# Optimization experiments

Measured on AMD Instinct MI355X. Metric: run time of the kernel, lower is better.

Reference implementation:

```python
import jax, jax.numpy as jnp
import numpy as np

N = 50000
E = 800000
IN_DIM = 128
HID = 32
HEADS = 4
OUT_DIM = 32
NEG_SLOPE = 0.2


def setup_inputs() -> dict:
    key = jax.random.key(0)
    ks = jax.random.split(key, 10)
    x = jax.random.normal(ks[0], (N, IN_DIM), dtype=jnp.float32)
    edge_index = jax.random.randint(ks[1], (2, E), 0, N, dtype=jnp.int64)
    # layer 1: in 128 -> 4 heads x 32, concat
    W1 = jax.random.normal(ks[2], (IN_DIM, HEADS * HID), dtype=jnp.float32) * (1.0 / np.sqrt(IN_DIM))
    a_src1 = jax.random.normal(ks[3], (HEADS, HID), dtype=jnp.float32) * 0.1
    a_dst1 = jax.random.normal(ks[4], (HEADS, HID), dtype=jnp.float32) * 0.1
    b1 = jnp.zeros((HEADS * HID,), dtype=jnp.float32)
    # layer 2: in 128 -> 1 head x 32, mean
    W2 = jax.random.normal(ks[5], (HEADS * HID, OUT_DIM), dtype=jnp.float32) * (1.0 / np.sqrt(HEADS * HID))
    a_src2 = jax.random.normal(ks[6], (1, OUT_DIM), dtype=jnp.float32) * 0.1
    a_dst2 = jax.random.normal(ks[7], (1, OUT_DIM), dtype=jnp.float32) * 0.1
    b2 = jnp.zeros((OUT_DIM,), dtype=jnp.float32)
    return {"x": x, "edge_index": edge_index, "W1": W1, "a_src1": a_src1,
            "a_dst1": a_dst1, "b1": b1, "W2": W2, "a_src2": a_src2,
            "a_dst2": a_dst2, "b2": b2}


def gat_layer(x, src, dst, W, a_src, a_dst, b, heads, concat, num_nodes):
    # linear transform -> [N, H, C]
    h = (x @ W).reshape(num_nodes, heads, -1)
    # per-node attention halves, gathered per edge -> [E, H]
    alpha = jax.nn.leaky_relu((h * a_src).sum(-1)[src] + (h * a_dst).sum(-1)[dst],
                              negative_slope=NEG_SLOPE)
    # segment softmax over edges grouped by destination node
    seg_max = jax.ops.segment_max(alpha, dst, num_segments=num_nodes)
    e = jnp.exp(alpha - seg_max[dst])
    denom = jax.ops.segment_sum(e, dst, num_segments=num_nodes)[dst]
    w = e / jnp.maximum(denom, 1e-16)
    # weighted message scatter-sum -> [N, H, C]
    out = jax.ops.segment_sum(h[src] * w[..., None], dst, num_segments=num_nodes)
    out = out.reshape(num_nodes, -1) if concat else out.mean(axis=1)
    return out + b


def reference(x, edge_index, W1, a_src1, a_dst1, b1, W2, a_src2, a_dst2, b2):
    num_nodes = x.shape[0]
    loops = jnp.arange(num_nodes, dtype=edge_index.dtype)
    src = jnp.concatenate([edge_index[0], loops])  # add self-loops (PyG default)
    dst = jnp.concatenate([edge_index[1], loops])
    h = jax.nn.relu(gat_layer(x, src, dst, W1, a_src1, a_dst1, b1, HEADS, True, num_nodes))
    out = gat_layer(h, src, dst, W2, a_src2, a_dst2, b2, 1, False, num_nodes)
    return jax.nn.sigmoid(out)
```

## Files before the change

kernel.cpp:

```cpp
#include <hip/hip_runtime.h>
#include <math.h>

#define NN 50000
#define NE 800000
#define NT (NN + NE)
#define SCAN_BLOCKS 196

__device__ __forceinline__ float lrelu(float a) { return a > 0.f ? a : 0.2f * a; }

__device__ __forceinline__ float sel4(float4 v, int h) {
  float r = v.x;
  r = (h == 1) ? v.y : r;
  r = (h == 2) ? v.z : r;
  r = (h == 3) ? v.w : r;
  return r;
}

__device__ __forceinline__ unsigned int f2bf(float f) {
  unsigned int u = __float_as_uint(f);
  return (u + 0x7FFFu + ((u >> 16) & 1u)) >> 16;
}
__device__ __forceinline__ unsigned int packbf(float lo, float hi) {
  return f2bf(lo) | (f2bf(hi) << 16);
}
__device__ __forceinline__ float bflo(unsigned int v) { return __uint_as_float(v << 16); }
__device__ __forceinline__ float bfhi(unsigned int v) { return __uint_as_float(v & 0xFFFF0000u); }

__global__ void k_detect(const unsigned int* __restrict__ eb, int* __restrict__ flag) {
  __shared__ int nz;
  if (threadIdx.x == 0) nz = 0;
  __syncthreads();
  int local = 0;
  for (int i = threadIdx.x; i < 2048; i += 256) local |= (eb[2 * i + 1] != 0u);
  if (local) nz = 1;
  __syncthreads();
  if (threadIdx.x == 0) *flag = (nz == 0) ? 1 : 0;
}

__global__ __launch_bounds__(256) void k_pass1(const void* __restrict__ eb,
                                               const int* __restrict__ flag,
                                               int* __restrict__ cnt,
                                               unsigned int* __restrict__ pw) {
  int e0 = (blockIdx.x * 256 + threadIdx.x) * 4;
  if (e0 >= NT) return;
  int is64 = *flag;
  int d0, d1, d2, d3;
  if (e0 < NE) {
    if (is64) {
      const uint4* p = (const uint4*)((const unsigned int*)eb + 2 * ((size_t)NE + e0));
      uint4 a = p[0], b = p[1];
      d0 = (int)a.x; d1 = (int)a.z; d2 = (int)b.x; d3 = (int)b.z;
    } else {
      int4 v = *(const int4*)((const int*)eb + (size_t)NE + e0);
      d0 = v.x; d1 = v.y; d2 = v.z; d3 = v.w;
    }
  } else {
    d0 = e0 - NE; d1 = d0 + 1; d2 = d0 + 2; d3 = d0 + 3;
  }
  unsigned int p0 = (unsigned int)atomicAdd(&cnt[d0], 1);
  unsigned int p1 = (unsigned int)atomicAdd(&cnt[d1], 1);
  unsigned int p2 = (unsigned int)atomicAdd(&cnt[d2], 1);
  unsigned int p3 = (unsigned int)atomicAdd(&cnt[d3], 1);
  *(uint4*)&pw[e0] = make_uint4(p0, p1, p2, p3);
}

__global__ __launch_bounds__(256) void k_bsum(const int* __restrict__ cnt,
                                              int* __restrict__ bsum) {
  int i = blockIdx.x * 256 + threadIdx.x;
  int v = (i < NN) ? cnt[i] : 0;
#pragma unroll
  for (int off = 1; off < 64; off <<= 1) v += __shfl_xor(v, off, 64);
  __shared__ int ws[4];
  int lane = threadIdx.x & 63, wid = threadIdx.x >> 6;
  if (lane == 0) ws[wid] = v;
  __syncthreads();
  if (threadIdx.x == 0) bsum[blockIdx.x] = ws[0] + ws[1] + ws[2] + ws[3];
}

__global__ __launch_bounds__(256) void k_bscan(const int* __restrict__ bsum,
                                               int* __restrict__ boff,
                                               int* __restrict__ rowp) {
  int t = threadIdx.x;
  int lane = t & 63, wid = t >> 6;
  int v = (t < SCAN_BLOCKS) ? bsum[t] : 0;
  int incl = v;
#pragma unroll
  for (int off = 1; off < 64; off <<= 1) {
    int u = __shfl_up(incl, off, 64);
    if (lane >= off) incl += u;
  }
  __shared__ int wsum[4], woff[4];
  if (lane == 63) wsum[wid] = incl;
  __syncthreads();
  if (t == 0) {
    woff[0] = 0;
    woff[1] = wsum[0];
    woff[2] = wsum[0] + wsum[1];
    woff[3] = wsum[0] + wsum[1] + wsum[2];
  }
  __syncthreads();
  if (t < SCAN_BLOCKS) boff[t] = woff[wid] + incl - v;
  if (t == 0) rowp[NN] = NT;
}

__global__ __launch_bounds__(256) void k_rowp(const int* __restrict__ cnt,
                                              const int* __restrict__ boff,
                                              int* __restrict__ rowp) {
  int i = blockIdx.x * 256 + threadIdx.x;
  int t = threadIdx.x;
  int lane = t & 63, wid = t >> 6;
  int v = (i < NN) ? cnt[i] : 0;
  int incl = v;
#pragma unroll
  for (int off = 1; off < 64; off <<= 1) {
    int u = __shfl_up(incl, off, 64);
    if (lane >= off) incl += u;
  }
  __shared__ int wsum[4], woff[4];
  if (lane == 63) wsum[wid] = incl;
  __syncthreads();
  if (t == 0) {
    woff[0] = 0;
    woff[1] = wsum[0];
    woff[2] = wsum[0] + wsum[1];
    woff[3] = wsum[0] + wsum[1] + wsum[2];
  }
  __syncthreads();
  if (i < NN) rowp[i] = boff[blockIdx.x] + woff[wid] + incl - v;
}

__global__ __launch_bounds__(256) void k_pass2(const void* __restrict__ eb,
                                               const int* __restrict__ flag,
                                               const int* __restrict__ rowp,
                                               const unsigned int* __restrict__ pw,
                                               int* __restrict__ csr) {
  int e0 = (blockIdx.x * 256 + threadIdx.x) * 4;
  if (e0 >= NT) return;
  int is64 = *flag;
  int s0, s1, s2, s3, d0, d1, d2, d3;
  if (e0 < NE) {
    if (is64) {
      const uint4* ps = (const uint4*)((const unsigned int*)eb + 2 * (size_t)e0);
      uint4 a = ps[0], b = ps[1];
      s0 = (int)a.x; s1 = (int)a.z; s2 = (int)b.x; s3 = (int)b.z;
      const uint4* pd = (const uint4*)((const unsigned int*)eb + 2 * ((size_t)NE + e0));
      uint4 c = pd[0], d = pd[1];
      d0 = (int)c.x; d1 = (int)c.z; d2 = (int)d.x; d3 = (int)d.z;
    } else {
      int4 vs = *(const int4*)((const int*)eb + (size_t)e0);
      s0 = vs.x; s1 = vs.y; s2 = vs.z; s3 = vs.w;
      int4 vd = *(const int4*)((const int*)eb + (size_t)NE + e0);
      d0 = vd.x; d1 = vd.y; d2 = vd.z; d3 = vd.w;
    }
  } else {
    s0 = d0 = e0 - NE;
    s1 = d1 = d0 + 1;
    s2 = d2 = d0 + 2;
    s3 = d3 = d0 + 3;
  }
  uint4 pv = *(const uint4*)&pw[e0];
  csr[rowp[d0] + (int)pv.x] = s0;
  csr[rowp[d1] + (int)pv.y] = s1;
  csr[rowp[d2] + (int)pv.z] = s2;
  csr[rowp[d3] + (int)pv.w] = s3;
}

__global__ __launch_bounds__(256) void k_gemm1(const float* __restrict__ X,
                                               const float* __restrict__ W,
                                               const float* __restrict__ a_src,
                                               const float* __restrict__ a_dst,
                                               unsigned int* __restrict__ Hb,
                                               float* __restrict__ AS,
                                               float* __restrict__ AD) {
  __shared__ float xt[32 * 36];
  __shared__ float wt[32 * 132];
  int tid = threadIdx.x;
  int tr = tid >> 6, tc = tid & 63;
  int r0 = blockIdx.x * 32;
  float acc[8][2];
#pragma unroll
  for (int i = 0; i < 8; ++i) {
    acc[i][0] = 0.f;
    acc[i][1] = 0.f;
  }

  for (int kb = 0; kb < 4; ++kb) {
    __syncthreads();
    {
      int row = tid >> 3, k4 = tid & 7;
      int gr = r0 + row;
      float4 v = make_float4(0.f, 0.f, 0.f, 0.f);
      if (gr < NN) v = ((const float4*)X)[(size_t)gr * 32 + kb * 8 + k4];
      xt[(k4 * 4 + 0) * 36 + row] = v.x;
      xt[(k4 * 4 + 1) * 36 + row] = v.y;
      xt[(k4 * 4 + 2) * 36 + row] = v.z;
      xt[(k4 * 4 + 3) * 36 + row] = v.w;
    }
#pragma unroll
    for (int i = tid; i < 1024; i += 256) {
      int kr = i >> 5, c4 = i & 31;
      *(float4*)&wt[kr * 132 + c4 * 4] = ((const float4*)W)[(size_t)(kb * 32 + kr) * 32 + c4];
    }
    __syncthreads();
#pragma unroll 4
    for (int k = 0; k < 32; ++k) {
      float4 xa = *(const float4*)&xt[k * 36 + tr * 8];
      float4 xb = *(const float4*)&xt[k * 36 + tr * 8 + 4];
      float2 wv = *(const float2*)&wt[k * 132 + tc * 2];
      float xr[8] = {xa.x, xa.y, xa.z, xa.w, xb.x, xb.y, xb.z, xb.w};
#pragma unroll
      for (int i = 0; i < 8; ++i) {
        acc[i][0] += xr[i] * wv.x;
        acc[i][1] += xr[i] * wv.y;
      }
    }
  }
  int head = tc >> 4;
  float2 sv = *(const float2*)&a_src[tc * 2];
  float2 dv = *(const float2*)&a_dst[tc * 2];
#pragma unroll
  for (int i = 0; i < 8; ++i) {
    int gr = r0 + tr * 8 + i;
    float ps = acc[i][0] * sv.x + acc[i][1] * sv.y;
    float pd = acc[i][0] * dv.x + acc[i][1] * dv.y;
#pragma unroll
    for (int off = 1; off < 16; off <<= 1) {
      ps += __shfl_xor(ps, off, 64);
      pd += __shfl_xor(pd, off, 64);
    }
    if (gr < NN) {
      Hb[(size_t)gr * 64 + tc] = packbf(acc[i][0], acc[i][1]);
      if ((tc & 15) == 0) {
        AS[gr * 4 + head] = ps;
        AD[gr * 4 + head] = pd;
      }
    }
  }
}

__global__ __launch_bounds__(256) void k_l1node(const int* __restrict__ rowp,
                                                const int* __restrict__ csr,
                                                const uint4* __restrict__ Hb,
                                                const float* __restrict__ AS,
                                                const float* __restrict__ AD,
                                                const float* __restrict__ b1,
                                                uint4* __restrict__ HMb) {
  int lane = threadIdx.x & 63, wid = threadIdx.x >> 6;
  int n = blockIdx.x * 4 + wid;
  if (n >= NN) return;
  int beg = rowp[n], end = rowp[n + 1];
  float4 ad4 = *(const float4*)&AD[n * 4];

  int sl = lane & 15;
  int g = lane >> 4;
  int hd = sl >> 2;
  float adh = sel4(ad4, hd);

  float a0 = 0.f, a1 = 0.f, a2 = 0.f, a3 = 0.f, a4 = 0.f, a5 = 0.f, a6 = 0.f, a7 = 0.f;
  float esum = 0.f;
  int i = beg + g;
  for (; i + 4 < end; i += 8) {
    int sA = csr[i];
    int sB = csr[i + 4];
    float lA = AS[sA * 4 + hd];
    float lB = AS[sB * 4 + hd];
    uint4 hA = Hb[(size_t)sA * 16 + sl];
    uint4 hB = Hb[(size_t)sB * 16 + sl];
    float wA = __expf(lrelu(lA + adh));
    float wB = __expf(lrelu(lB + adh));
    esum += wA + wB;
    a0 += wA * bflo(hA.x) + wB * bflo(hB.x);
    a1 += wA * bfhi(hA.x) + wB * bfhi(hB.x);
    a2 += wA * bflo(hA.y) + wB * bflo(hB.y);
    a3 += wA * bfhi(hA.y) + wB * bfhi(hB.y);
    a4 += wA * bflo(hA.z) + wB * bflo(hB.z);
    a5 += wA * bfhi(hA.z) + wB * bfhi(hB.z);
    a6 += wA * bflo(hA.w) + wB * bflo(hB.w);
    a7 += wA * bfhi(hA.w) + wB * bfhi(hB.w);
  }
  if (i < end) {
    int s = csr[i];
    float l = AS[s * 4 + hd];
    uint4 hv = Hb[(size_t)s * 16 + sl];
    float w0 = __expf(lrelu(l + adh));
    esum += w0;
    a0 += w0 * bflo(hv.x);
    a1 += w0 * bfhi(hv.x);
    a2 += w0 * bflo(hv.y);
    a3 += w0 * bfhi(hv.y);
    a4 += w0 * bflo(hv.z);
    a5 += w0 * bfhi(hv.z);
    a6 += w0 * bflo(hv.w);
    a7 += w0 * bfhi(hv.w);
  }
#pragma unroll
  for (int off = 16; off < 64; off <<= 1) {
    esum += __shfl_xor(esum, off, 64);
    a0 += __shfl_xor(a0, off, 64);
    a1 += __shfl_xor(a1, off, 64);
    a2 += __shfl_xor(a2, off, 64);
    a3 += __shfl_xor(a3, off, 64);
    a4 += __shfl_xor(a4, off, 64);
    a5 += __shfl_xor(a5, off, 64);
    a6 += __shfl_xor(a6, off, 64);
    a7 += __shfl_xor(a7, off, 64);
  }
  if (lane < 16) {
    float r = 1.f / esum;
    int c = sl * 8;
    float4 bva = *(const float4*)&b1[c];
    float4 bvb = *(const float4*)&b1[c + 4];
    float v0 = fmaxf(a0 * r + bva.x, 0.f);
    float v1 = fmaxf(a1 * r + bva.y, 0.f);
    float v2 = fmaxf(a2 * r + bva.z, 0.f);
    float v3 = fmaxf(a3 * r + bva.w, 0.f);
    float v4 = fmaxf(a4 * r + bvb.x, 0.f);
    float v5 = fmaxf(a5 * r + bvb.y, 0.f);
    float v6 = fmaxf(a6 * r + bvb.z, 0.f);
    float v7 = fmaxf(a7 * r + bvb.w, 0.f);
    HMb[(size_t)n * 16 + sl] =
        make_uint4(packbf(v0, v1), packbf(v2, v3), packbf(v4, v5), packbf(v6, v7));
  }
}

__global__ __launch_bounds__(256) void k_gemm2(const uint4* __restrict__ HMb,
                                               const float* __restrict__ W2,
                                               const float* __restrict__ a_src2,
                                               const float* __restrict__ a_dst2,
                                               uint4* __restrict__ Hb2,
                                               float* __restrict__ AS,
                                               float* __restrict__ AD) {
  __shared__ float wsm[128 * 32];
  int tid = threadIdx.x;
  for (int i = tid; i < 1024; i += 256) ((float4*)wsm)[i] = ((const float4*)W2)[i];
  __syncthreads();
  int rl = tid >> 2, sub = tid & 3;
  int r = blockIdx.x * 64 + rl;
  float acc[32];
#pragma unroll
  for (int j = 0; j < 32; ++j) acc[j] = 0.f;

  if (r < NN) {
    const uint4* xp = &HMb[(size_t)r * 16 + sub * 4];
    uint4 xq0 = xp[0], xq1 = xp[1], xq2 = xp[2], xq3 = xp[3];
    int kbase = sub * 32;
    unsigned int wds[16] = {xq0.x, xq0.y, xq0.z, xq0.w, xq1.x, xq1.y, xq1.z, xq1.w,
                            xq2.x, xq2.y, xq2.z, xq2.w, xq3.x, xq3.y, xq3.z, xq3.w};
#pragma unroll
    for (int t = 0; t < 16; ++t) {
      float xlo = bflo(wds[t]);
      float xhi = bfhi(wds[t]);
      const float4* wr0 = (const float4*)&wsm[(kbase + t * 2) * 32];
      const float4* wr1 = (const float4*)&wsm[(kbase + t * 2 + 1) * 32];
#pragma unroll
      for (int j4 = 0; j4 < 8; ++j4) {
        float4 w0 = wr0[j4];
        float4 w1 = wr1[j4];
        acc[j4 * 4 + 0] += xlo * w0.x + xhi * w1.x;
        acc[j4 * 4 + 1] += xlo * w0.y + xhi * w1.y;
        acc[j4 * 4 + 2] += xlo * w0.z + xhi * w1.z;
        acc[j4 * 4 + 3] += xlo * w0.w + xhi * w1.w;
      }
    }
  }
#pragma unroll
  for (int j = 0; j < 32; ++j) {
    acc[j] += __shfl_xor(acc[j], 1, 64);
    acc[j] += __shfl_xor(acc[j], 2, 64);
  }
  if (r < NN) {
    int c = sub * 8;
    float4 sv0 = ((const float4*)a_src2)[sub * 2];
    float4 sv1 = ((const float4*)a_src2)[sub * 2 + 1];
    float4 dv0 = ((const float4*)a_dst2)[sub * 2];
    float4 dv1 = ((const float4*)a_dst2)[sub * 2 + 1];
    float ps = acc[c + 0] * sv0.x + acc[c + 1] * sv0.y + acc[c + 2] * sv0.z +
               acc[c + 3] * sv0.w + acc[c + 4] * sv1.x + acc[c + 5] * sv1.y +
               acc[c + 6] * sv1.z + acc[c + 7] * sv1.w;
    float pd = acc[c + 0] * dv0.x + acc[c + 1] * dv0.y + acc[c + 2] * dv0.z +
               acc[c + 3] * dv0.w + acc[c + 4] * dv1.x + acc[c + 5] * dv1.y +
               acc[c + 6] * dv1.z + acc[c + 7] * dv1.w;
    ps += __shfl_xor(ps, 1, 64);
    ps += __shfl_xor(ps, 2, 64);
    pd += __shfl_xor(pd, 1, 64);
    pd += __shfl_xor(pd, 2, 64);
    Hb2[(size_t)r * 4 + sub] =
        make_uint4(packbf(acc[c + 0], acc[c + 1]), packbf(acc[c + 2], acc[c + 3]),
                   packbf(acc[c + 4], acc[c + 5]), packbf(acc[c + 6], acc[c + 7]));
    if (sub == 0) {
      AS[r] = ps;
      AD[r] = pd;
    }
  }
}

__global__ __launch_bounds__(256) void k_l2node(const int* __restrict__ rowp,
                                                const int* __restrict__ csr,
                                                const uint2* __restrict__ Hb2,
                                                const float* __restrict__ AS,
                                                const float* __restrict__ AD,
                                                const float* __restrict__ b2,
                                                float* __restrict__ out) {
  int lane = threadIdx.x & 63, wid = threadIdx.x >> 6;
  int n = blockIdx.x * 4 + wid;
  if (n >= NN) return;
  int beg = rowp[n], end = rowp[n + 1];
  float adn = AD[n];

  int sl = lane & 7;
  int g = lane >> 3;
  float a0 = 0.f, a1 = 0.f, a2 = 0.f, a3 = 0.f;
  float esum = 0.f;
  int i = beg + g;
  for (; i + 8 < end; i += 16) {
    int sA = csr[i];
    int sB = csr[i + 8];
    float lA = AS[sA];
    float lB = AS[sB];
    uint2 hA = Hb2[(size_t)sA * 8 + sl];
    uint2 hB = Hb2[(size_t)sB * 8 + sl];
    float wA = __expf(lrelu(lA + adn));
    float wB = __expf(lrelu(lB + adn));
    esum += wA + wB;
    a0 += wA * bflo(hA.x) + wB * bflo(hB.x);
    a1 += wA * bfhi(hA.x) + wB * bfhi(hB.x);
    a2 += wA * bflo(hA.y) + wB * bflo(hB.y);
    a3 += wA * bfhi(hA.y) + wB * bfhi(hB.y);
  }
  if (i < end) {
    int s = csr[i];
    float l = AS[s];
    uint2 hv = Hb2[(size_t)s * 8 + sl];
    float w0 = __expf(lrelu(l + adn));
    esum += w0;
    a0 += w0 * bflo(hv.x);
    a1 += w0 * bfhi(hv.x);
    a2 += w0 * bflo(hv.y);
    a3 += w0 * bfhi(hv.y);
  }
#pragma unroll
  for (int off = 8; off < 64; off <<= 1) {
    esum += __shfl_xor(esum, off, 64);
    a0 += __shfl_xor(a0, off, 64);
    a1 += __shfl_xor(a1, off, 64);
    a2 += __shfl_xor(a2, off, 64);
    a3 += __shfl_xor(a3, off, 64);
  }
  if (lane < 8) {
    float r = 1.f / esum;
    int c = sl * 4;
    float4 bv = *(const float4*)&b2[c];
    float vx = a0 * r + bv.x, vy = a1 * r + bv.y, vz = a2 * r + bv.z, vw = a3 * r + bv.w;
    *(float4*)&out[(size_t)n * 32 + c] =
        make_float4(1.f / (1.f + __expf(-vx)), 1.f / (1.f + __expf(-vy)),
                    1.f / (1.f + __expf(-vz)), 1.f / (1.f + __expf(-vw)));
  }
}

extern "C" void kernel_launch(void* const* d_in, const int* in_sizes, int n_in,
                              void* d_out, int out_size, void* d_ws, size_t ws_size,
                              hipStream_t stream) {
  (void)in_sizes; (void)n_in; (void)out_size; (void)ws_size;
  const float* x      = (const float*)d_in[0];
  const void*  eb     = d_in[1];
  const float* W1     = (const float*)d_in[2];
  const float* a_src1 = (const float*)d_in[3];
  const float* a_dst1 = (const float*)d_in[4];
  const float* b1     = (const float*)d_in[5];
  const float* W2     = (const float*)d_in[6];
  const float* a_src2 = (const float*)d_in[7];
  const float* a_dst2 = (const float*)d_in[8];
  const float* b2     = (const float*)d_in[9];
  float* out = (float*)d_out;

  char* w = (char*)d_ws;
  auto alloc = [&](size_t bytes) {
    char* p = w;
    w += (bytes + 255) & ~(size_t)255;
    return p;
  };
  int*          flag = (int*)alloc(4);
  int*          cnt  = (int*)alloc((size_t)NN * 4);
  int*          rowp = (int*)alloc((size_t)(NN + 1) * 4);
  unsigned int* pw   = (unsigned int*)alloc((size_t)NT * 4);
  int*          csr  = (int*)alloc((size_t)NT * 4);
  int*          bsum = (int*)alloc((size_t)SCAN_BLOCKS * 4);
  int*          boff = (int*)alloc((size_t)SCAN_BLOCKS * 4);
  uint4*        Hb1  = (uint4*)alloc((size_t)NN * 128 * 2);
  float*        AS1  = (float*)alloc((size_t)NN * 16);
  float*        AD1  = (float*)alloc((size_t)NN * 16);
  uint4*        HMb  = (uint4*)alloc((size_t)NN * 128 * 2);
  uint4* Hb2 = Hb1;
  float* AS2 = (float*)cnt;
  float* AD2 = (float*)pw;

  hipMemsetAsync(cnt, 0, (size_t)NN * 4, stream);
  k_detect<<<1, 256, 0, stream>>>((const unsigned int*)eb, flag);
  int egrid4 = (NT / 4 + 255) / 256;
  k_pass1<<<egrid4, 256, 0, stream>>>(eb, flag, cnt, pw);
  k_bsum<<<SCAN_BLOCKS, 256, 0, stream>>>(cnt, bsum);
  k_bscan<<<1, 256, 0, stream>>>(bsum, boff, rowp);
  k_rowp<<<SCAN_BLOCKS, 256, 0, stream>>>(cnt, boff, rowp);
  k_pass2<<<egrid4, 256, 0, stream>>>(eb, flag, rowp, pw, csr);

  k_gemm1<<<(NN + 31) / 32, 256, 0, stream>>>(x, W1, a_src1, a_dst1,
                                              (unsigned int*)Hb1, AS1, AD1);
  k_l1node<<<(NN + 3) / 4, 256, 0, stream>>>(rowp, csr, Hb1, AS1, AD1, b1, HMb);
  k_gemm2<<<(NN + 63) / 64, 256, 0, stream>>>(HMb, W2, a_src2, a_dst2, Hb2, AS2, AD2);
  k_l2node<<<(NN + 3) / 4, 256, 0, stream>>>(rowp, csr, (const uint2*)Hb2, AS2, AD2, b2, out);
}
```

Baseline: 275.1 us.

## Fuse layer-2 projection into layer-1 aggregation and drop detect/scan launches

The layer-1 neighbour aggregation kernel now also does the layer-2 linear transform and attention dot products in-wave, using W2 staged in shared memory. This removes the k_gemm2 launch and the full bf16 round-trip of the hidden activations through global memory. The separate edge-dtype detect kernel is replaced by a per-wave ballot probe inside the edge passes, and the single-block block-offset scan is folded into k_rowp, which cuts two more launches. In exchange, every 4-node block reloads the 16 KB W2 into LDS, which adds heavy redundant L2 traffic and LDS pressure and may limit occupancy.

```diff
diff --git a/kernel.cpp b/kernel.cpp
--- a/kernel.cpp
+++ b/kernel.cpp
@@ -26,26 +26,21 @@
 __device__ __forceinline__ float bflo(unsigned int v) { return __uint_as_float(v << 16); }
 __device__ __forceinline__ float bfhi(unsigned int v) { return __uint_as_float(v & 0xFFFF0000u); }
 
-__global__ void k_detect(const unsigned int* __restrict__ eb, int* __restrict__ flag) {
-  __shared__ int nz;
-  if (threadIdx.x == 0) nz = 0;
-  __syncthreads();
-  int local = 0;
-  for (int i = threadIdx.x; i < 2048; i += 256) local |= (eb[2 * i + 1] != 0u);
-  if (local) nz = 1;
-  __syncthreads();
-  if (threadIdx.x == 0) *flag = (nz == 0) ? 1 : 0;
+__device__ __forceinline__ int wave_is64(const void* eb, int wbase, int lane) {
+  unsigned int probe = ((const unsigned int*)eb)[2 * (size_t)(wbase + lane) + 1];
+  return (__ballot(probe != 0u) == 0ULL) ? 1 : 0;
 }
 
 __global__ __launch_bounds__(256) void k_pass1(const void* __restrict__ eb,
-                                               const int* __restrict__ flag,
                                                int* __restrict__ cnt,
                                                unsigned int* __restrict__ pw) {
   int e0 = (blockIdx.x * 256 + threadIdx.x) * 4;
   if (e0 >= NT) return;
-  int is64 = *flag;
+  int lane = threadIdx.x & 63;
   int d0, d1, d2, d3;
   if (e0 < NE) {
+    int wbase = (blockIdx.x * 256 + (threadIdx.x & ~63)) * 4;
+    int is64 = wave_is64(eb, wbase, lane);
     if (is64) {
       const uint4* p = (const uint4*)((const unsigned int*)eb + 2 * ((size_t)NE + e0));
       uint4 a = p[0], b = p[1];
@@ -77,68 +72,67 @@
   if (threadIdx.x == 0) bsum[blockIdx.x] = ws[0] + ws[1] + ws[2] + ws[3];
 }
 
-__global__ __launch_bounds__(256) void k_bscan(const int* __restrict__ bsum,
-                                               int* __restrict__ boff,
-                                               int* __restrict__ rowp) {
+__global__ __launch_bounds__(256) void k_rowp(const int* __restrict__ cnt,
+                                              const int* __restrict__ bsum,
+                                              int* __restrict__ rowp) {
+  __shared__ int pref[256];
+  __shared__ int wsum1[4], woff1[4];
   int t = threadIdx.x;
   int lane = t & 63, wid = t >> 6;
-  int v = (t < SCAN_BLOCKS) ? bsum[t] : 0;
+  {
+    int v = (t < SCAN_BLOCKS) ? bsum[t] : 0;
+    int incl = v;
+#pragma unroll
+    for (int off = 1; off < 64; off <<= 1) {
+      int u = __shfl_up(incl, off, 64);
+      if (lane >= off) incl += u;
+    }
+    if (lane == 63) wsum1[wid] = incl;
+    __syncthreads();
+    if (t == 0) {
+      woff1[0] = 0;
+      woff1[1] = wsum1[0];
+      woff1[2] = wsum1[0] + wsum1[1];
+      woff1[3] = wsum1[0] + wsum1[1] + wsum1[2];
+    }
+    __syncthreads();
+    pref[t] = woff1[wid] + incl - v;
+    __syncthreads();
+  }
+  int boffb = pref[blockIdx.x];
+  __shared__ int wsum2[4], woff2[4];
+  int i = blockIdx.x * 256 + t;
+  int v = (i < NN) ? cnt[i] : 0;
   int incl = v;
 #pragma unroll
   for (int off = 1; off < 64; off <<= 1) {
     int u = __shfl_up(incl, off, 64);
     if (lane >= off) incl += u;
   }
-  __shared__ int wsum[4], woff[4];
-  if (lane == 63) wsum[wid] = incl;
+  if (lane == 63) wsum2[wid] = incl;
   __syncthreads();
   if (t == 0) {
-    woff[0] = 0;
-    woff[1] = wsum[0];
-    woff[2] = wsum[0] + wsum[1];
-    woff[3] = wsum[0] + wsum[1] + wsum[2];
+    woff2[0] = 0;
+    woff2[1] = wsum2[0];
+    woff2[2] = wsum2[0] + wsum2[1];
+    woff2[3] = wsum2[0] + wsum2[1] + wsum2[2];
   }
   __syncthreads();
-  if (t < SCAN_BLOCKS) boff[t] = woff[wid] + incl - v;
-  if (t == 0) rowp[NN] = NT;
-}
-
-__global__ __launch_bounds__(256) void k_rowp(const int* __restrict__ cnt,
-                                              const int* __restrict__ boff,
-                                              int* __restrict__ rowp) {
-  int i = blockIdx.x * 256 + threadIdx.x;
-  int t = threadIdx.x;
-  int lane = t & 63, wid = t >> 6;
-  int v = (i < NN) ? cnt[i] : 0;
-  int incl = v;
-#pragma unroll
-  for (int off = 1; off < 64; off <<= 1) {
-    int u = __shfl_up(incl, off, 64);
-    if (lane >= off) incl += u;
-  }
-  __shared__ int wsum[4], woff[4];
-  if (lane == 63) wsum[wid] = incl;
-  __syncthreads();
-  if (t == 0) {
-    woff[0] = 0;
-    woff[1] = wsum[0];
-    woff[2] = wsum[0] + wsum[1];
-    woff[3] = wsum[0] + wsum[1] + wsum[2];
-  }
-  __syncthreads();
-  if (i < NN) rowp[i] = boff[blockIdx.x] + woff[wid] + incl - v;
+  if (i < NN) rowp[i] = boffb + woff2[wid] + incl - v;
+  if (blockIdx.x == 0 && t == 0) rowp[NN] = NT;
 }
 
 __global__ __launch_bounds__(256) void k_pass2(const void* __restrict__ eb,
-                                               const int* __restrict__ flag,
                                                const int* __restrict__ rowp,
                                                const unsigned int* __restrict__ pw,
                                                int* __restrict__ csr) {
   int e0 = (blockIdx.x * 256 + threadIdx.x) * 4;
   if (e0 >= NT) return;
-  int is64 = *flag;
+  int lane = threadIdx.x & 63;
   int s0, s1, s2, s3, d0, d1, d2, d3;
   if (e0 < NE) {
+    int wbase = (blockIdx.x * 256 + (threadIdx.x & ~63)) * 4;
+    int is64 = wave_is64(eb, wbase, lane);
     if (is64) {
       const uint4* ps = (const uint4*)((const unsigned int*)eb + 2 * (size_t)e0);
       uint4 a = ps[0], b = ps[1];
@@ -238,14 +232,24 @@
   }
 }
 
-__global__ __launch_bounds__(256) void k_l1node(const int* __restrict__ rowp,
-                                                const int* __restrict__ csr,
-                                                const uint4* __restrict__ Hb,
-                                                const float* __restrict__ AS,
-                                                const float* __restrict__ AD,
-                                                const float* __restrict__ b1,
-                                                uint4* __restrict__ HMb) {
-  int lane = threadIdx.x & 63, wid = threadIdx.x >> 6;
+__global__ __launch_bounds__(256) void k_l1g2(const int* __restrict__ rowp,
+                                              const int* __restrict__ csr,
+                                              const uint4* __restrict__ Hb,
+                                              const float* __restrict__ AS,
+                                              const float* __restrict__ AD,
+                                              const float* __restrict__ b1,
+                                              const float* __restrict__ W2,
+                                              const float* __restrict__ as2,
+                                              const float* __restrict__ ad2,
+                                              uint4* __restrict__ Hb2,
+                                              float* __restrict__ AS2,
+                                              float* __restrict__ AD2) {
+  __shared__ float wsm[128 * 32];
+  int tid = threadIdx.x;
+  for (int i = tid; i < 1024; i += 256) ((float4*)wsm)[i] = ((const float4*)W2)[i];
+  __syncthreads();
+
+  int lane = tid & 63, wid = tid >> 6;
   int n = blockIdx.x * 4 + wid;
   if (n >= NN) return;
   int beg = rowp[n], end = rowp[n + 1];
@@ -305,92 +309,68 @@
     a6 += __shfl_xor(a6, off, 64);
     a7 += __shfl_xor(a7, off, 64);
   }
-  if (lane < 16) {
-    float r = 1.f / esum;
-    int c = sl * 8;
-    float4 bva = *(const float4*)&b1[c];
-    float4 bvb = *(const float4*)&b1[c + 4];
-    float v0 = fmaxf(a0 * r + bva.x, 0.f);
-    float v1 = fmaxf(a1 * r + bva.y, 0.f);
-    float v2 = fmaxf(a2 * r + bva.z, 0.f);
-    float v3 = fmaxf(a3 * r + bva.w, 0.f);
-    float v4 = fmaxf(a4 * r + bvb.x, 0.f);
-    float v5 = fmaxf(a5 * r + bvb.y, 0.f);
-    float v6 = fmaxf(a6 * r + bvb.z, 0.f);
-    float v7 = fmaxf(a7 * r + bvb.w, 0.f);
-    HMb[(size_t)n * 16 + sl] =
-        make_uint4(packbf(v0, v1), packbf(v2, v3), packbf(v4, v5), packbf(v6, v7));
-  }
-}
-
-__global__ __launch_bounds__(256) void k_gemm2(const uint4* __restrict__ HMb,
-                                               const float* __restrict__ W2,
-                                               const float* __restrict__ a_src2,
-                                               const float* __restrict__ a_dst2,
-                                               uint4* __restrict__ Hb2,
-                                               float* __restrict__ AS,
-                                               float* __restrict__ AD) {
-  __shared__ float wsm[128 * 32];
-  int tid = threadIdx.x;
-  for (int i = tid; i < 1024; i += 256) ((float4*)wsm)[i] = ((const float4*)W2)[i];
-  __syncthreads();
-  int rl = tid >> 2, sub = tid & 3;
-  int r = blockIdx.x * 64 + rl;
-  float acc[32];
-#pragma unroll
-  for (int j = 0; j < 32; ++j) acc[j] = 0.f;
-
-  if (r < NN) {
-    const uint4* xp = &HMb[(size_t)r * 16 + sub * 4];
-    uint4 xq0 = xp[0], xq1 = xp[1], xq2 = xp[2], xq3 = xp[3];
-    int kbase = sub * 32;
-    unsigned int wds[16] = {xq0.x, xq0.y, xq0.z, xq0.w, xq1.x, xq1.y, xq1.z, xq1.w,
-                            xq2.x, xq2.y, xq2.z, xq2.w, xq3.x, xq3.y, xq3.z, xq3.w};
-#pragma unroll
-    for (int t = 0; t < 16; ++t) {
-      float xlo = bflo(wds[t]);
-      float xhi = bfhi(wds[t]);
-      const float4* wr0 = (const float4*)&wsm[(kbase + t * 2) * 32];
-      const float4* wr1 = (const float4*)&wsm[(kbase + t * 2 + 1) * 32];
-#pragma unroll
-      for (int j4 = 0; j4 < 8; ++j4) {
-        float4 w0 = wr0[j4];
-        float4 w1 = wr1[j4];
-        acc[j4 * 4 + 0] += xlo * w0.x + xhi * w1.x;
-        acc[j4 * 4 + 1] += xlo * w0.y + xhi * w1.y;
-        acc[j4 * 4 + 2] += xlo * w0.z + xhi * w1.z;
-        acc[j4 * 4 + 3] += xlo * w0.w + xhi * w1.w;
-      }
-    }
-  }
-#pragma unroll
-  for (int j = 0; j < 32; ++j) {
-    acc[j] += __shfl_xor(acc[j], 1, 64);
-    acc[j] += __shfl_xor(acc[j], 2, 64);
-  }
-  if (r < NN) {
-    int c = sub * 8;
-    float4 sv0 = ((const float4*)a_src2)[sub * 2];
-    float4 sv1 = ((const float4*)a_src2)[sub * 2 + 1];
-    float4 dv0 = ((const float4*)a_dst2)[sub * 2];
-    float4 dv1 = ((const float4*)a_dst2)[sub * 2 + 1];
-    float ps = acc[c + 0] * sv0.x + acc[c + 1] * sv0.y + acc[c + 2] * sv0.z +
-               acc[c + 3] * sv0.w + acc[c + 4] * sv1.x + acc[c + 5] * sv1.y +
-               acc[c + 6] * sv1.z + acc[c + 7] * sv1.w;
-    float pd = acc[c + 0] * dv0.x + acc[c + 1] * dv0.y + acc[c + 2] * dv0.z +
-               acc[c + 3] * dv0.w + acc[c + 4] * dv1.x + acc[c + 5] * dv1.y +
-               acc[c + 6] * dv1.z + acc[c + 7] * dv1.w;
-    ps += __shfl_xor(ps, 1, 64);
-    ps += __shfl_xor(ps, 2, 64);
-    pd += __shfl_xor(pd, 1, 64);
-    pd += __shfl_xor(pd, 2, 64);
-    Hb2[(size_t)r * 4 + sub] =
-        make_uint4(packbf(acc[c + 0], acc[c + 1]), packbf(acc[c + 2], acc[c + 3]),
-                   packbf(acc[c + 4], acc[c + 5]), packbf(acc[c + 6], acc[c + 7]));
-    if (sub == 0) {
-      AS[r] = ps;
-      AD[r] = pd;
-    }
+  float r = 1.f / esum;
+  int c = sl * 8;
+  float4 bva = *(const float4*)&b1[c];
+  float4 bvb = *(const float4*)&b1[c + 4];
+  float v[8];
+  v[0] = fmaxf(a0 * r + bva.x, 0.f);
+  v[1] = fmaxf(a1 * r + bva.y, 0.f);
+  v[2] = fmaxf(a2 * r + bva.z, 0.f);
+  v[3] = fmaxf(a3 * r + bva.w, 0.f);
+  v[4] = fmaxf(a4 * r + bvb.x, 0.f);
+  v[5] = fmaxf(a5 * r + bvb.y, 0.f);
+  v[6] = fmaxf(a6 * r + bvb.z, 0.f);
+  v[7] = fmaxf(a7 * r + bvb.w, 0.f);
+
+  int jb = g * 8;
+  float p[8] = {0.f, 0.f, 0.f, 0.f, 0.f, 0.f, 0.f, 0.f};
+#pragma unroll
+  for (int t = 0; t < 8; ++t) {
+    int k = sl * 8 + t;
+    float vt = v[t];
+    float4 wA = *(const float4*)&wsm[k * 32 + jb];
+    float4 wB = *(const float4*)&wsm[k * 32 + jb + 4];
+    p[0] += vt * wA.x;
+    p[1] += vt * wA.y;
+    p[2] += vt * wA.z;
+    p[3] += vt * wA.w;
+    p[4] += vt * wB.x;
+    p[5] += vt * wB.y;
+    p[6] += vt * wB.z;
+    p[7] += vt * wB.w;
+  }
+#pragma unroll
+  for (int off = 1; off < 16; off <<= 1) {
+    p[0] += __shfl_xor(p[0], off, 64);
+    p[1] += __shfl_xor(p[1], off, 64);
+    p[2] += __shfl_xor(p[2], off, 64);
+    p[3] += __shfl_xor(p[3], off, 64);
+    p[4] += __shfl_xor(p[4], off, 64);
+    p[5] += __shfl_xor(p[5], off, 64);
+    p[6] += __shfl_xor(p[6], off, 64);
+    p[7] += __shfl_xor(p[7], off, 64);
+  }
+  float4 s2a = *(const float4*)&as2[jb];
+  float4 s2b = *(const float4*)&as2[jb + 4];
+  float4 d2a = *(const float4*)&ad2[jb];
+  float4 d2b = *(const float4*)&ad2[jb + 4];
+  float ps = p[0] * s2a.x + p[1] * s2a.y + p[2] * s2a.z + p[3] * s2a.w +
+             p[4] * s2b.x + p[5] * s2b.y + p[6] * s2b.z + p[7] * s2b.w;
+  float pd = p[0] * d2a.x + p[1] * d2a.y + p[2] * d2a.z + p[3] * d2a.w +
+             p[4] * d2b.x + p[5] * d2b.y + p[6] * d2b.z + p[7] * d2b.w;
+  ps += __shfl_xor(ps, 16, 64);
+  ps += __shfl_xor(ps, 32, 64);
+  pd += __shfl_xor(pd, 16, 64);
+  pd += __shfl_xor(pd, 32, 64);
+
+  if (sl == 0) {
+    Hb2[(size_t)n * 4 + g] = make_uint4(packbf(p[0], p[1]), packbf(p[2], p[3]),
+                                        packbf(p[4], p[5]), packbf(p[6], p[7]));
+  }
+  if (lane == 0) {
+    AS2[n] = ps;
+    AD2[n] = pd;
   }
 }
 
@@ -479,33 +459,29 @@
     w += (bytes + 255) & ~(size_t)255;
     return p;
   };
-  int*          flag = (int*)alloc(4);
   int*          cnt  = (int*)alloc((size_t)NN * 4);
   int*          rowp = (int*)alloc((size_t)(NN + 1) * 4);
   unsigned int* pw   = (unsigned int*)alloc((size_t)NT * 4);
   int*          csr  = (int*)alloc((size_t)NT * 4);
   int*          bsum = (int*)alloc((size_t)SCAN_BLOCKS * 4);
-  int*          boff = (int*)alloc((size_t)SCAN_BLOCKS * 4);
   uint4*        Hb1  = (uint4*)alloc((size_t)NN * 128 * 2);
   float*        AS1  = (float*)alloc((size_t)NN * 16);
   float*        AD1  = (float*)alloc((size_t)NN * 16);
-  uint4*        HMb  = (uint4*)alloc((size_t)NN * 128 * 2);
-  uint4* Hb2 = Hb1;
+  uint4*        Hb2  = (uint4*)alloc((size_t)NN * 32 * 2);
   float* AS2 = (float*)cnt;
   float* AD2 = (float*)pw;
 
   hipMemsetAsync(cnt, 0, (size_t)NN * 4, stream);
-  k_detect<<<1, 256, 0, stream>>>((const unsigned int*)eb, flag);
   int egrid4 = (NT / 4 + 255) / 256;
-  k_pass1<<<egrid4, 256, 0, stream>>>(eb, flag, cnt, pw);
+  k_pass1<<<egrid4, 256, 0, stream>>>(eb, cnt, pw);
   k_bsum<<<SCAN_BLOCKS, 256, 0, stream>>>(cnt, bsum);
-  k_bscan<<<1, 256, 0, stream>>>(bsum, boff, rowp);
-  k_rowp<<<SCAN_BLOCKS, 256, 0, stream>>>(cnt, boff, rowp);
-  k_pass2<<<egrid4, 256, 0, stream>>>(eb, flag, rowp, pw, csr);
+  k_rowp<<<SCAN_BLOCKS, 256, 0, stream>>>(cnt, bsum, rowp);
+  k_pass2<<<egrid4, 256, 0, stream>>>(eb, rowp, pw, csr);
 
   k_gemm1<<<(NN + 31) / 32, 256, 0, stream>>>(x, W1, a_src1, a_dst1,
                                               (unsigned int*)Hb1, AS1, AD1);
-  k_l1node<<<(NN + 3) / 4, 256, 0, stream>>>(rowp, csr, Hb1, AS1, AD1, b1, HMb);
-  k_gemm2<<<(NN + 63) / 64, 256, 0, stream>>>(HMb, W2, a_src2, a_dst2, Hb2, AS2, AD2);
-  k_l2node<<<(NN + 3) / 4, 256, 0, stream>>>(rowp, csr, (const uint2*)Hb2, AS2, AD2, b2, out);
-}
+  k_l1g2<<<(NN + 3) / 4, 256, 0, stream>>>(rowp, csr, Hb1, AS1, AD1, b1, W2,
+                                           a_src2, a_dst2, Hb2, AS2, AD2);
+  k_l2node<<<(NN + 3) / 4, 256, 0, stream>>>(rowp, csr, (const uint2*)Hb2, AS2, AD2,
+                                             b2, out);
+}
```

New measurement: 284.2 us. 3.3% more time.
